# Kernel tuning notes

Measured on AMD Instinct MI355X. Metric: run time of the kernel, lower is better.

The kernel has to match this reference:

```python
import jax, jax.numpy as jnp
import numpy as np

WEIGHTS = (1.0, 2.0, 3.0, 4.0)  # first 4 entries of [1,2,3,4,5,1] for our 4 scales


def _nearest_downsample(pl, H, W):
    # pl: (B,1,H0,W0) int labels; PyTorch F.interpolate nearest: src = floor(dst*H0/H)
    B, _, H0, W0 = pl.shape
    ih = (jnp.arange(H) * H0) // H
    iw = (jnp.arange(W) * W0) // W
    return pl[:, 0][:, ih][:, :, iw]  # (B,H,W)


def _per_class_kl_mean(labels, feat, feat_old, num_class):
    # labels: (N,) int; feat, feat_old: (N,C). Returns (num_class,) per-class mean KL,
    # 0 for absent classes. Labels >= num_class (e.g. 255 ignore) are dropped,
    # matching the original's removal of the 255 class.
    logp = jax.nn.log_softmax(feat, axis=1)
    logq = jax.nn.log_softmax(feat_old, axis=1)
    kl_pix = jnp.sum(jnp.exp(logp) * (logp - logq), axis=1)  # (N,)
    valid = labels < num_class
    seg = jnp.where(valid, labels, num_class)  # invalid -> dummy bucket
    sums = jax.ops.segment_sum(jnp.where(valid, kl_pix, 0.0), seg,
                               num_segments=num_class + 1)[:num_class]
    cnts = jax.ops.segment_sum(valid.astype(feat.dtype), seg,
                               num_segments=num_class + 1)[:num_class]
    return jnp.where(cnts > 0, sums / jnp.maximum(cnts, 1.0), 0.0)


def _forward(pseudo_labels, feats_new, feats_old, num_class, num_old_class):
    cls = jnp.arange(num_class)
    # cl==0 -> num_old/num, 1<=cl<=num_old -> 1, else 0 (absent classes give 0 mean anyway)
    coef = jnp.where(cls == 0, float(num_old_class) / float(num_class),
                     jnp.where(cls <= num_old_class, 1.0, 0.0)).astype(jnp.float32)
    loss = jnp.float32(0.0)
    for idx, (f_new, f_old) in enumerate(zip(feats_new, feats_old)):
        B, C, H, W = f_new.shape
        pl = _nearest_downsample(pseudo_labels, H, W).reshape(-1)  # (B*H*W,)
        feat = jnp.transpose(f_new, (0, 2, 3, 1)).reshape(-1, C)   # (BHW, C)
        feat_old = jnp.transpose(f_old, (0, 2, 3, 1)).reshape(-1, C)
        mean_kl = _per_class_kl_mean(pl, feat, feat_old, num_class)
        loss = loss + WEIGHTS[idx] * jnp.sum(coef * mean_kl)
    return loss


def setup_inputs() -> dict:
    key = jax.random.key(0)
    ks = jax.random.split(key, 9)
    B = 8
    shapes = [(B, 256, 128, 128), (B, 512, 64, 64), (B, 1024, 32, 32), (B, 2048, 16, 16)]
    inp = {}
    inp["pseudo_labels"] = jax.random.randint(ks[0], (B, 1, 512, 512), 0, 21, dtype=jnp.int32)
    for i, s in enumerate(shapes):
        inp[f"feat_new_{i}"] = jax.random.normal(ks[1 + i], s, dtype=jnp.float32)
        inp[f"feat_old_{i}"] = jax.random.normal(ks[5 + i], s, dtype=jnp.float32)
    inp["num_class"] = 21
    inp["num_old_class"] = 15
    return inp


def reference(pseudo_labels, feat_new_0, feat_new_1, feat_new_2, feat_new_3,
              feat_old_0, feat_old_1, feat_old_2, feat_old_3,
              num_class, num_old_class):
    feats_new = (feat_new_0, feat_new_1, feat_new_2, feat_new_3)
    feats_old = (feat_old_0, feat_old_1, feat_old_2, feat_old_3)
    return _forward(pseudo_labels, feats_new, feats_old, num_class, num_old_class)
```

## Files before the change

kernel.cpp:

```cpp
#include <hip/hip_runtime.h>
#include <cstdint>
#include <cstddef>


#define TPB 256

#define P3 2048
#define WS_ZERO_FLOATS (P3 * 3 + 256)

__global__ __launch_bounds__(TPB)
void k0_zero(float* __restrict__ ws) {
    const int i = blockIdx.x * TPB + threadIdx.x;
    if (i < WS_ZERO_FLOATS) ws[i] = 0.f;
}

template<int C, int HW, int W, int F, int PIXT, int CG, int SPLIT>
__device__ __forceinline__ void scale_pass(const float* __restrict__ fn,
                                           const float* __restrict__ fo,
                                           const int* __restrict__ labels,
                                           int ncls, int sc,
                                           float* __restrict__ pZn,
                                           float* __restrict__ pZo,
                                           float* __restrict__ pS,
                                           float* __restrict__ clsSum,
                                           float* __restrict__ clsCnt,
                                           float* red, float* ls, float* lc,
                                           int lb) {
    constexpr int PIXB = 4 * PIXT;
    constexpr int NPB  = (8 * HW) / PIXB;
    constexpr int CH   = C / SPLIT;
    constexpr int IT   = CH / CG;

    const int t  = threadIdx.x;
    const int tx = t % PIXT;
    const int ty = t / PIXT;
    const int pb = lb % NPB;
    const int sp = lb / NPB;

    const int q0 = pb * PIXB;
    const int b  = q0 / HW;
    const int p  = (q0 % HW) + tx * 4;
    const size_t base = (size_t)b * C * HW + p;
    const float* bn = fn + base;
    const float* bo = fo + base;
    const int cbase = sp * CH;

    float zn0=0.f, zn1=0.f, zn2=0.f, zn3=0.f;
    float zo0=0.f, zo1=0.f, zo2=0.f, zo3=0.f;
    float s0 =0.f, s1 =0.f, s2 =0.f, s3 =0.f;

    for (int k = 0; k < IT; ++k) {
        const int c = cbase + k * CG + ty;
        const float4 xn = *(const float4*)(bn + (size_t)c * HW);
        const float4 xo = *(const float4*)(bo + (size_t)c * HW);
        float en, eo;
        en = __expf(xn.x); eo = __expf(xo.x);
        zn0 += en; zo0 += eo; s0 += en * (xn.x - xo.x);
        en = __expf(xn.y); eo = __expf(xo.y);
        zn1 += en; zo1 += eo; s1 += en * (xn.y - xo.y);
        en = __expf(xn.z); eo = __expf(xo.z);
        zn2 += en; zo2 += eo; s2 += en * (xn.z - xo.z);
        en = __expf(xn.w); eo = __expf(xo.w);
        zn3 += en; zo3 += eo; s3 += en * (xn.w - xo.w);
    }

    float* r = red + (size_t)(ty * PIXT + tx) * 12;
    r[0]  = zn0; r[1]  = zo0; r[2]  = s0;
    r[3]  = zn1; r[4]  = zo1; r[5]  = s1;
    r[6]  = zn2; r[7]  = zo2; r[8]  = s2;
    r[9]  = zn3; r[10] = zo3; r[11] = s3;
    if (t < 32) { ls[t] = 0.f; lc[t] = 0.f; }
    __syncthreads();

    for (int i = t; i < PIXB; i += TPB) {
        const int txi = i >> 2;
        const int j   = i & 3;
        float zn = 0.f, zo = 0.f, s = 0.f;
        #pragma unroll
        for (int g = 0; g < CG; ++g) {
            const float* rr = red + (size_t)(g * PIXT + txi) * 12 + j * 3;
            zn += rr[0]; zo += rr[1]; s += rr[2];
        }
        const int q = q0 + i;
        if (SPLIT == 1) {
            const float kl = s / zn - logf(zn) + logf(zo);
            const int pp = q % HW;
            const int h  = pp / W;
            const int w  = pp % W;
            const int lab = labels[b * 262144 + (h * F) * 512 + (w * F)];
            if ((unsigned)lab < (unsigned)ncls) {
                atomicAdd(&ls[lab], kl);
                atomicAdd(&lc[lab], 1.0f);
            }
        } else {
            atomicAdd(&pZn[q], zn);
            atomicAdd(&pZo[q], zo);
            atomicAdd(&pS[q],  s);
        }
    }

    if (SPLIT == 1) {
        __syncthreads();
        if (t < 32) {
            const float cv = lc[t];
            if (cv != 0.f) {
                atomicAdd(&clsSum[sc * 32 + t], ls[t]);
                atomicAdd(&clsCnt[sc * 32 + t], cv);
            }
        }
    }
}

__global__ __launch_bounds__(TPB)
void k1_fused(const float* __restrict__ fn0, const float* __restrict__ fo0,
              const float* __restrict__ fn1, const float* __restrict__ fo1,
              const float* __restrict__ fn2, const float* __restrict__ fo2,
              const float* __restrict__ fn3, const float* __restrict__ fo3,
              const int* __restrict__ labels, const int* __restrict__ pNC,
              float* __restrict__ pZn, float* __restrict__ pZo,
              float* __restrict__ pS,
              float* __restrict__ clsSum, float* __restrict__ clsCnt) {
    __shared__ float red[TPB * 12];
    __shared__ float ls[32], lc[32];
    const int ncls = *pNC;
    const int bb = blockIdx.x;
    if (bb < 512) {
        scale_pass<256, 16384, 128, 4, 64, 4, 1>(fn0, fo0, labels, ncls, 0,
            pZn, pZo, pS, clsSum, clsCnt, red, ls, lc, bb);
    } else if (bb < 768) {
        scale_pass<512, 4096, 64, 8, 32, 8, 1>(fn1, fo1, labels, ncls, 1,
            pZn, pZo, pS, clsSum, clsCnt, red, ls, lc, bb - 512);
    } else if (bb < 1024) {
        scale_pass<1024, 1024, 32, 16, 8, 32, 1>(fn2, fo2, labels, ncls, 2,
            pZn, pZo, pS, clsSum, clsCnt, red, ls, lc, bb - 768);
    } else {
        scale_pass<2048, 256, 16, 32, 8, 32, 4>(fn3, fo3, labels, ncls, 3,
            pZn, pZo, pS, clsSum, clsCnt, red, ls, lc, bb - 1024);
    }
}

__global__ __launch_bounds__(TPB)
void k2_scale3(const int* __restrict__ labels,
               const float* __restrict__ pZn, const float* __restrict__ pZo,
               const float* __restrict__ pS,
               float* __restrict__ clsSum, float* __restrict__ clsCnt,
               const int* __restrict__ pNC) {
    const int ncls = *pNC;
    const int t = threadIdx.x;
    const int q = blockIdx.x * TPB + t;
    __shared__ float ls[32], lc[32];
    if (t < 32) { ls[t] = 0.f; lc[t] = 0.f; }
    __syncthreads();
    const float zn = pZn[q];
    const float zo = pZo[q];
    const float s  = pS[q];
    const float kl = s / zn - logf(zn) + logf(zo);
    const int b  = q / 256;
    const int pp = q % 256;
    const int h  = pp / 16;
    const int w  = pp % 16;
    const int lab = labels[b * 262144 + (h * 32) * 512 + (w * 32)];
    if ((unsigned)lab < (unsigned)ncls) {
        atomicAdd(&ls[lab], kl);
        atomicAdd(&lc[lab], 1.0f);
    }
    __syncthreads();
    if (t < 32 && lc[t] != 0.f) {
        atomicAdd(&clsSum[96 + t], ls[t]);
        atomicAdd(&clsCnt[96 + t], lc[t]);
    }
}

__global__ void k3_finalize(const float* __restrict__ clsSum,
                            const float* __restrict__ clsCnt,
                            const int* __restrict__ pNC,
                            const int* __restrict__ pNOC,
                            float* __restrict__ out) {
    const int t = threadIdx.x;
    const int ncls = *pNC;
    const int nold = *pNOC;
    float acc = 0.f;
    for (int i = t; i < 128; i += 64) {
        const int s_ = i / 32;
        const int c  = i % 32;
        if (c < ncls) {
            const float cnt = clsCnt[i];
            const float sum = clsSum[i];
            const float mean = (cnt > 0.f) ? (sum / cnt) : 0.f;
            const float coef = (c == 0) ? (float)nold / (float)ncls
                                        : ((c <= nold) ? 1.f : 0.f);
            acc += (float)(s_ + 1) * coef * mean;
        }
    }
    #pragma unroll
    for (int off = 32; off > 0; off >>= 1) acc += __shfl_down(acc, off, 64);
    if (t == 0) out[0] = acc;
}

extern "C" void kernel_launch(void* const* d_in, const int* in_sizes, int n_in,
                              void* d_out, int out_size, void* d_ws, size_t ws_size,
                              hipStream_t stream) {
    const int* labels = (const int*)d_in[0];
    const int* pNC;
    const int* pNOC;
    const float* fn[4];
    const float* fo[4];

    if (in_sizes[2] == in_sizes[1]) {
        fn[0] = (const float*)d_in[1]; fo[0] = (const float*)d_in[2];
        fn[1] = (const float*)d_in[3]; fo[1] = (const float*)d_in[4];
        fn[2] = (const float*)d_in[5]; fo[2] = (const float*)d_in[6];
        fn[3] = (const float*)d_in[7]; fo[3] = (const float*)d_in[8];
    } else {
        fn[0] = (const float*)d_in[1]; fn[1] = (const float*)d_in[2];
        fn[2] = (const float*)d_in[3]; fn[3] = (const float*)d_in[4];
        fo[0] = (const float*)d_in[5]; fo[1] = (const float*)d_in[6];
        fo[2] = (const float*)d_in[7]; fo[3] = (const float*)d_in[8];
    }
    pNC  = (const int*)d_in[9];
    pNOC = (const int*)d_in[10];

    float* ws = (float*)d_ws;
    float* pZn = ws;
    float* pZo = ws + P3;
    float* pS  = ws + 2 * P3;
    float* clsSum = ws + 3 * P3;
    float* clsCnt = clsSum + 128;

    k0_zero<<<(WS_ZERO_FLOATS + TPB - 1) / TPB, TPB, 0, stream>>>(ws);
    k1_fused<<<1280, TPB, 0, stream>>>(fn[0], fo[0], fn[1], fo[1],
                                       fn[2], fo[2], fn[3], fo[3],
                                       labels, pNC, pZn, pZo, pS, clsSum, clsCnt);
    k2_scale3<<<P3 / TPB, TPB, 0, stream>>>(labels, pZn, pZo, pS, clsSum, clsCnt, pNC);
    k3_finalize<<<1, 64, 0, stream>>>(clsSum, clsCnt, pNC, pNOC, (float*)d_out);
}
```

Before: 113.1 us.

## Stream feature tiles via global_load_lds double buffering with per-wave channel groups

Rewrites the main reduction pass so each wave asynchronously loads 8-channel by 64-pixel tiles of both feature maps directly into LDS with global_load_lds, double-buffered and synchronised with explicit waitcnt, then consumes them from LDS. The work split changes to per-wave channel groups. Block order is reordered so the heavy small-spatial scales run first, scale 3 uses a 2-way channel split, and the grid grows to 1728 blocks with a 4-blocks-per-CU launch bound. The intent is to keep more memory requests in flight and hide load latency on this bandwidth-bound pass, at the cost of 32KB of LDS per block and hand-written wait counts that could be fragile.

```diff
diff --git a/kernel.cpp b/kernel.cpp
--- a/kernel.cpp
+++ b/kernel.cpp
@@ -4,9 +4,12 @@
 
 
 #define TPB 256
-
 #define P3 2048
 #define WS_ZERO_FLOATS (P3 * 3 + 256)
+
+#define GLL16(gp, lp) __builtin_amdgcn_global_load_lds(                        \
+    (const __attribute__((address_space(1))) unsigned int*)(gp),               \
+    (__attribute__((address_space(3))) unsigned int*)(lp), 16, 0, 0)
 
 __global__ __launch_bounds__(TPB)
 void k0_zero(float* __restrict__ ws) {
@@ -14,7 +17,7 @@
     if (i < WS_ZERO_FLOATS) ws[i] = 0.f;
 }
 
-template<int C, int HW, int W, int F, int PIXT, int CG, int SPLIT>
+template<int C, int HW, int W, int F, int NPGRP, int WCH, int SPLIT>
 __device__ __forceinline__ void scale_pass(const float* __restrict__ fn,
                                            const float* __restrict__ fo,
                                            const int* __restrict__ labels,
@@ -24,94 +27,134 @@
                                            float* __restrict__ pS,
                                            float* __restrict__ clsSum,
                                            float* __restrict__ clsCnt,
-                                           float* red, float* ls, float* lc,
-                                           int lb) {
-    constexpr int PIXB = 4 * PIXT;
-    constexpr int NPB  = (8 * HW) / PIXB;
-    constexpr int CH   = C / SPLIT;
-    constexpr int IT   = CH / CG;
-
-    const int t  = threadIdx.x;
-    const int tx = t % PIXT;
-    const int ty = t / PIXT;
+                                           float* smem, int lb) {
+    constexpr int NPIX = NPGRP * 64;
+    constexpr int NPB  = (8 * HW) / NPIX;
+    constexpr int NCK  = WCH / 8;
+    constexpr int NCHG = 4 / NPGRP;
+
+    const int tid  = threadIdx.x;
+    const int wid  = tid >> 6;
+    const int lane = tid & 63;
     const int pb = lb % NPB;
     const int sp = lb / NPB;
 
-    const int q0 = pb * PIXB;
-    const int b  = q0 / HW;
-    const int p  = (q0 % HW) + tx * 4;
-    const size_t base = (size_t)b * C * HW + p;
-    const float* bn = fn + base;
-    const float* bo = fo + base;
-    const int cbase = sp * CH;
-
-    float zn0=0.f, zn1=0.f, zn2=0.f, zn3=0.f;
-    float zo0=0.f, zo1=0.f, zo2=0.f, zo3=0.f;
-    float s0 =0.f, s1 =0.f, s2 =0.f, s3 =0.f;
-
-    for (int k = 0; k < IT; ++k) {
-        const int c = cbase + k * CG + ty;
-        const float4 xn = *(const float4*)(bn + (size_t)c * HW);
-        const float4 xo = *(const float4*)(bo + (size_t)c * HW);
-        float en, eo;
-        en = __expf(xn.x); eo = __expf(xo.x);
-        zn0 += en; zo0 += eo; s0 += en * (xn.x - xo.x);
-        en = __expf(xn.y); eo = __expf(xo.y);
-        zn1 += en; zo1 += eo; s1 += en * (xn.y - xo.y);
-        en = __expf(xn.z); eo = __expf(xo.z);
-        zn2 += en; zo2 += eo; s2 += en * (xn.z - xo.z);
-        en = __expf(xn.w); eo = __expf(xo.w);
-        zn3 += en; zo3 += eo; s3 += en * (xn.w - xo.w);
-    }
-
-    float* r = red + (size_t)(ty * PIXT + tx) * 12;
-    r[0]  = zn0; r[1]  = zo0; r[2]  = s0;
-    r[3]  = zn1; r[4]  = zo1; r[5]  = s1;
-    r[6]  = zn2; r[7]  = zo2; r[8]  = s2;
-    r[9]  = zn3; r[10] = zo3; r[11] = s3;
-    if (t < 32) { ls[t] = 0.f; lc[t] = 0.f; }
-    __syncthreads();
-
-    for (int i = t; i < PIXB; i += TPB) {
-        const int txi = i >> 2;
-        const int j   = i & 3;
+    const int pg = wid % NPGRP;
+    const int cg = wid / NPGRP;
+
+    const int blkpix0 = pb * NPIX;
+    const int p0 = blkpix0 + pg * 64;
+    const int b  = p0 / HW;
+    const int ppix = p0 % HW;
+    const int ch0w = sp * (NCHG * WCH) + cg * WCH;
+
+    const int cst = lane >> 4;
+    const int qq  = lane & 15;
+
+    const float* gn = fn + ((size_t)b * C + ch0w + cst) * HW + ppix + qq * 4;
+    const float* go = fo + ((size_t)b * C + ch0w + cst) * HW + ppix + qq * 4;
+
+    float* wbuf = smem + wid * 2048;
+
+    float zn0=0.f,zn1=0.f,zn2=0.f,zn3=0.f;
+    float zo0=0.f,zo1=0.f,zo2=0.f,zo3=0.f;
+    float sA0=0.f,sA1=0.f,sA2=0.f,sA3=0.f;
+
+#define STAGE(k_, d_) do {                                                     \
+        const size_t co_ = (size_t)((k_) * 8) * HW;                            \
+        float* lb0_ = wbuf + (d_) * 1024;                                      \
+        GLL16(gn + co_,              lb0_);                                    \
+        GLL16(gn + co_ + 4 * (size_t)HW, lb0_ + 256);                          \
+        GLL16(go + co_,              lb0_ + 512);                              \
+        GLL16(go + co_ + 4 * (size_t)HW, lb0_ + 768);                          \
+    } while (0)
+
+#define ACC(nv, ov, i_) { const float en_=__expf(nv), eo_=__expf(ov);          \
+        zn##i_ += en_; zo##i_ += eo_; sA##i_ += en_ * ((nv) - (ov)); }
+
+#define CONSUME(d_) do {                                                       \
+        const float* nb_ = wbuf + (d_) * 1024;                                 \
+        const float* ob_ = nb_ + 512;                                          \
+        const float4 n0_ = *(const float4*)(nb_ + (2*cst  )*64 + qq*4);        \
+        const float4 n1_ = *(const float4*)(nb_ + (2*cst+1)*64 + qq*4);        \
+        const float4 o0_ = *(const float4*)(ob_ + (2*cst  )*64 + qq*4);        \
+        const float4 o1_ = *(const float4*)(ob_ + (2*cst+1)*64 + qq*4);        \
+        ACC(n0_.x,o0_.x,0) ACC(n0_.y,o0_.y,1) ACC(n0_.z,o0_.z,2) ACC(n0_.w,o0_.w,3) \
+        ACC(n1_.x,o1_.x,0) ACC(n1_.y,o1_.y,1) ACC(n1_.z,o1_.z,2) ACC(n1_.w,o1_.w,3) \
+    } while (0)
+
+    STAGE(0, 0);
+    STAGE(1, 1);
+    for (int k = 0; k < NCK - 1; ++k) {
+        asm volatile("s_waitcnt vmcnt(4)" ::: "memory");
+        __builtin_amdgcn_sched_barrier(0);
+        CONSUME(k & 1);
+        asm volatile("s_waitcnt lgkmcnt(0)" ::: "memory");
+        __builtin_amdgcn_sched_barrier(0);
+        if (k + 2 < NCK) STAGE(k + 2, k & 1);
+    }
+    asm volatile("s_waitcnt vmcnt(0)" ::: "memory");
+    __builtin_amdgcn_sched_barrier(0);
+    CONSUME((NCK - 1) & 1);
+
+#undef STAGE
+#undef ACC
+#undef CONSUME
+
+    __syncthreads();
+    float* red = smem;
+    float* r = red + tid * 12;
+    r[0]=zn0; r[1]=zn1; r[2]=zn2;  r[3]=zn3;
+    r[4]=zo0; r[5]=zo1; r[6]=zo2;  r[7]=zo3;
+    r[8]=sA0; r[9]=sA1; r[10]=sA2; r[11]=sA3;
+    float* ls = smem + 3072;
+    float* lc = smem + 3104;
+    if (tid < 32) { ls[tid] = 0.f; lc[tid] = 0.f; }
+    __syncthreads();
+
+    for (int i = tid; i < NPIX; i += TPB) {
+        const int Q = i >> 2, j = i & 3;
+        const int pgq = (NPGRP == 2) ? (Q >> 4) : 0;
+        const int ql = Q & 15;
         float zn = 0.f, zo = 0.f, s = 0.f;
         #pragma unroll
-        for (int g = 0; g < CG; ++g) {
-            const float* rr = red + (size_t)(g * PIXT + txi) * 12 + j * 3;
-            zn += rr[0]; zo += rr[1]; s += rr[2];
-        }
-        const int q = q0 + i;
+        for (int cgi = 0; cgi < NCHG; ++cgi) {
+            #pragma unroll
+            for (int g = 0; g < 4; ++g) {
+                const float* rr = red + ((pgq + cgi * NPGRP) * 64 + g * 16 + ql) * 12;
+                zn += rr[j]; zo += rr[4 + j]; s += rr[8 + j];
+            }
+        }
+        const int qg = blkpix0 + i;
         if (SPLIT == 1) {
             const float kl = s / zn - logf(zn) + logf(zo);
-            const int pp = q % HW;
-            const int h  = pp / W;
-            const int w  = pp % W;
+            const int pp = qg % HW;
+            const int h = pp / W, w = pp % W;
             const int lab = labels[b * 262144 + (h * F) * 512 + (w * F)];
             if ((unsigned)lab < (unsigned)ncls) {
                 atomicAdd(&ls[lab], kl);
                 atomicAdd(&lc[lab], 1.0f);
             }
         } else {
-            atomicAdd(&pZn[q], zn);
-            atomicAdd(&pZo[q], zo);
-            atomicAdd(&pS[q],  s);
+            atomicAdd(&pZn[qg], zn);
+            atomicAdd(&pZo[qg], zo);
+            atomicAdd(&pS[qg],  s);
         }
     }
 
     if (SPLIT == 1) {
         __syncthreads();
-        if (t < 32) {
-            const float cv = lc[t];
+        if (tid < 32) {
+            const float cv = lc[tid];
             if (cv != 0.f) {
-                atomicAdd(&clsSum[sc * 32 + t], ls[t]);
-                atomicAdd(&clsCnt[sc * 32 + t], cv);
+                atomicAdd(&clsSum[sc * 32 + tid], ls[tid]);
+                atomicAdd(&clsCnt[sc * 32 + tid], cv);
             }
         }
     }
 }
 
-__global__ __launch_bounds__(TPB)
+__global__ __launch_bounds__(TPB, 4)
 void k1_fused(const float* __restrict__ fn0, const float* __restrict__ fo0,
               const float* __restrict__ fn1, const float* __restrict__ fo1,
               const float* __restrict__ fn2, const float* __restrict__ fo2,
@@ -120,22 +163,21 @@
               float* __restrict__ pZn, float* __restrict__ pZo,
               float* __restrict__ pS,
               float* __restrict__ clsSum, float* __restrict__ clsCnt) {
-    __shared__ float red[TPB * 12];
-    __shared__ float ls[32], lc[32];
+    __shared__ float smem[8192];
     const int ncls = *pNC;
     const int bb = blockIdx.x;
-    if (bb < 512) {
-        scale_pass<256, 16384, 128, 4, 64, 4, 1>(fn0, fo0, labels, ncls, 0,
-            pZn, pZo, pS, clsSum, clsCnt, red, ls, lc, bb);
-    } else if (bb < 768) {
-        scale_pass<512, 4096, 64, 8, 32, 8, 1>(fn1, fo1, labels, ncls, 1,
-            pZn, pZo, pS, clsSum, clsCnt, red, ls, lc, bb - 512);
-    } else if (bb < 1024) {
-        scale_pass<1024, 1024, 32, 16, 8, 32, 1>(fn2, fo2, labels, ncls, 2,
-            pZn, pZo, pS, clsSum, clsCnt, red, ls, lc, bb - 768);
+    if (bb < 128) {
+        scale_pass<1024, 1024, 32, 16, 1, 256, 1>(fn2, fo2, labels, ncls, 2,
+            pZn, pZo, pS, clsSum, clsCnt, smem, bb);
+    } else if (bb < 192) {
+        scale_pass<2048, 256, 16, 32, 1, 256, 2>(fn3, fo3, labels, ncls, 3,
+            pZn, pZo, pS, clsSum, clsCnt, smem, bb - 128);
+    } else if (bb < 704) {
+        scale_pass<512, 4096, 64, 8, 1, 128, 1>(fn1, fo1, labels, ncls, 1,
+            pZn, pZo, pS, clsSum, clsCnt, smem, bb - 192);
     } else {
-        scale_pass<2048, 256, 16, 32, 8, 32, 4>(fn3, fo3, labels, ncls, 3,
-            pZn, pZo, pS, clsSum, clsCnt, red, ls, lc, bb - 1024);
+        scale_pass<256, 16384, 128, 4, 2, 128, 1>(fn0, fo0, labels, ncls, 0,
+            pZn, pZo, pS, clsSum, clsCnt, smem, bb - 704);
     }
 }
 
@@ -201,8 +243,6 @@
                               void* d_out, int out_size, void* d_ws, size_t ws_size,
                               hipStream_t stream) {
     const int* labels = (const int*)d_in[0];
-    const int* pNC;
-    const int* pNOC;
     const float* fn[4];
     const float* fo[4];
 
@@ -217,8 +257,8 @@
         fo[0] = (const float*)d_in[5]; fo[1] = (const float*)d_in[6];
         fo[2] = (const float*)d_in[7]; fo[3] = (const float*)d_in[8];
     }
-    pNC  = (const int*)d_in[9];
-    pNOC = (const int*)d_in[10];
+    const int* pNC  = (const int*)d_in[9];
+    const int* pNOC = (const int*)d_in[10];
 
     float* ws = (float*)d_ws;
     float* pZn = ws;
@@ -228,7 +268,7 @@
     float* clsCnt = clsSum + 128;
 
     k0_zero<<<(WS_ZERO_FLOATS + TPB - 1) / TPB, TPB, 0, stream>>>(ws);
-    k1_fused<<<1280, TPB, 0, stream>>>(fn[0], fo[0], fn[1], fo[1],
+    k1_fused<<<1728, TPB, 0, stream>>>(fn[0], fo[0], fn[1], fo[1],
                                        fn[2], fo[2], fn[3], fo[3],
                                        labels, pNC, pZn, pZo, pS, clsSum, clsCnt);
     k2_scale3<<<P3 / TPB, TPB, 0, stream>>>(labels, pZn, pZo, pS, clsSum, clsCnt, pNC);
```

Result: faster. 107.8 us (-4.7%).

## Use uniform 256-pixel x 256-channel tiles with split-channel atomics for scales 1-3

Applied to the files above, without the earlier changes.

Every scale now uses the same block tile: 256 pixels by 256 channels, four waves of 64 channels each, with loads unrolled four channels deep. Scales 1 and 2 now split channels across blocks too, and partial softmax sums go to a larger global partial buffer through atomics. A generalized second kernel then finishes scales 1-3, and launch bounds request 4 blocks per CU. The aim is uniform memory-level parallelism and fewer reduction stalls, at the cost of more global atomics and a larger workspace to zero.

```diff
diff --git a/kernel.cpp b/kernel.cpp
--- a/kernel.cpp
+++ b/kernel.cpp
@@ -4,9 +4,10 @@
 
 
 #define TPB 256
-
-#define P3 2048
-#define WS_ZERO_FLOATS (P3 * 3 + 256)
+#define NPART 43008
+#define WS_ZERO_FLOATS (NPART * 3 + 256)
+
+#define LD4(p) (*(const float4*)(p))
 
 __global__ __launch_bounds__(TPB)
 void k0_zero(float* __restrict__ ws) {
@@ -14,104 +15,100 @@
     if (i < WS_ZERO_FLOATS) ws[i] = 0.f;
 }
 
-template<int C, int HW, int W, int F, int PIXT, int CG, int SPLIT>
+template<int C, int HW, int W, int F, bool FIN>
 __device__ __forceinline__ void scale_pass(const float* __restrict__ fn,
                                            const float* __restrict__ fo,
                                            const int* __restrict__ labels,
-                                           int ncls, int sc,
+                                           int ncls, int pOff,
                                            float* __restrict__ pZn,
                                            float* __restrict__ pZo,
                                            float* __restrict__ pS,
                                            float* __restrict__ clsSum,
                                            float* __restrict__ clsCnt,
-                                           float* red, float* ls, float* lc,
-                                           int lb) {
-    constexpr int PIXB = 4 * PIXT;
-    constexpr int NPB  = (8 * HW) / PIXB;
-    constexpr int CH   = C / SPLIT;
-    constexpr int IT   = CH / CG;
-
-    const int t  = threadIdx.x;
-    const int tx = t % PIXT;
-    const int ty = t / PIXT;
-    const int pb = lb % NPB;
-    const int sp = lb / NPB;
-
-    const int q0 = pb * PIXB;
-    const int b  = q0 / HW;
-    const int p  = (q0 % HW) + tx * 4;
-    const size_t base = (size_t)b * C * HW + p;
-    const float* bn = fn + base;
-    const float* bo = fo + base;
-    const int cbase = sp * CH;
-
-    float zn0=0.f, zn1=0.f, zn2=0.f, zn3=0.f;
-    float zo0=0.f, zo1=0.f, zo2=0.f, zo3=0.f;
-    float s0 =0.f, s1 =0.f, s2 =0.f, s3 =0.f;
-
-    for (int k = 0; k < IT; ++k) {
-        const int c = cbase + k * CG + ty;
-        const float4 xn = *(const float4*)(bn + (size_t)c * HW);
-        const float4 xo = *(const float4*)(bo + (size_t)c * HW);
-        float en, eo;
-        en = __expf(xn.x); eo = __expf(xo.x);
-        zn0 += en; zo0 += eo; s0 += en * (xn.x - xo.x);
-        en = __expf(xn.y); eo = __expf(xo.y);
-        zn1 += en; zo1 += eo; s1 += en * (xn.y - xo.y);
-        en = __expf(xn.z); eo = __expf(xo.z);
-        zn2 += en; zo2 += eo; s2 += en * (xn.z - xo.z);
-        en = __expf(xn.w); eo = __expf(xo.w);
-        zn3 += en; zo3 += eo; s3 += en * (xn.w - xo.w);
-    }
-
-    float* r = red + (size_t)(ty * PIXT + tx) * 12;
-    r[0]  = zn0; r[1]  = zo0; r[2]  = s0;
-    r[3]  = zn1; r[4]  = zo1; r[5]  = s1;
-    r[6]  = zn2; r[7]  = zo2; r[8]  = s2;
-    r[9]  = zn3; r[10] = zo3; r[11] = s3;
-    if (t < 32) { ls[t] = 0.f; lc[t] = 0.f; }
+                                           float* smem, int lb) {
+    constexpr int NPXB = (8 * HW) / 256;
+
+    const int tid  = threadIdx.x;
+    const int wid  = tid >> 6;
+    const int lane = tid & 63;
+    const int pxb = lb % NPXB;
+    const int cb  = lb / NPXB;
+
+    const int q0  = pxb * 256;
+    const int b   = q0 / HW;
+    const int px0 = q0 % HW;
+    const int c0  = cb * 256 + wid * 64;
+
+    const float* pn = fn + ((size_t)b * C + c0) * HW + px0 + 4 * lane;
+    const float* po = fo + ((size_t)b * C + c0) * HW + px0 + 4 * lane;
+
+    float zn0=0.f,zn1=0.f,zn2=0.f,zn3=0.f;
+    float zo0=0.f,zo1=0.f,zo2=0.f,zo3=0.f;
+    float sA0=0.f,sA1=0.f,sA2=0.f,sA3=0.f;
+
+#define ACC(nv, ov, i_) { const float en_=__expf(nv), eo_=__expf(ov);          \
+        zn##i_ += en_; zo##i_ += eo_; sA##i_ += en_ * ((nv) - (ov)); }
+#define ACCQ(a_, b_) { ACC(a_.x,b_.x,0) ACC(a_.y,b_.y,1)                        \
+                       ACC(a_.z,b_.z,2) ACC(a_.w,b_.w,3) }
+
+    for (int k = 0; k < 64; k += 4) {
+        const size_t o0 = (size_t)(k + 0) * HW;
+        const size_t o1 = (size_t)(k + 1) * HW;
+        const size_t o2 = (size_t)(k + 2) * HW;
+        const size_t o3 = (size_t)(k + 3) * HW;
+        const float4 xn0 = LD4(pn + o0), xn1 = LD4(pn + o1);
+        const float4 xn2 = LD4(pn + o2), xn3 = LD4(pn + o3);
+        const float4 xo0 = LD4(po + o0), xo1 = LD4(po + o1);
+        const float4 xo2 = LD4(po + o2), xo3 = LD4(po + o3);
+        ACCQ(xn0, xo0) ACCQ(xn1, xo1) ACCQ(xn2, xo2) ACCQ(xn3, xo3)
+    }
+#undef ACC
+#undef ACCQ
+
+    float* lacc = smem;
+    float* r = lacc + wid * 768 + lane * 12;
+    r[0]=zn0; r[1]=zo0; r[2]=sA0;
+    r[3]=zn1; r[4]=zo1; r[5]=sA1;
+    r[6]=zn2; r[7]=zo2; r[8]=sA2;
+    r[9]=zn3; r[10]=zo3; r[11]=sA3;
+    float* ls = smem + 3072;
+    float* lc = smem + 3104;
+    if (tid < 32) { ls[tid] = 0.f; lc[tid] = 0.f; }
     __syncthreads();
 
-    for (int i = t; i < PIXB; i += TPB) {
-        const int txi = i >> 2;
-        const int j   = i & 3;
-        float zn = 0.f, zo = 0.f, s = 0.f;
-        #pragma unroll
-        for (int g = 0; g < CG; ++g) {
-            const float* rr = red + (size_t)(g * PIXT + txi) * 12 + j * 3;
-            zn += rr[0]; zo += rr[1]; s += rr[2];
+    float zn = 0.f, zo = 0.f, s = 0.f;
+    #pragma unroll
+    for (int w = 0; w < 4; ++w) {
+        const float* rr = lacc + w * 768 + tid * 3;
+        zn += rr[0]; zo += rr[1]; s += rr[2];
+    }
+
+    if (FIN) {
+        const float kl = s / zn - logf(zn) + logf(zo);
+        const int pp = px0 + tid;
+        const int h = pp / W, w = pp % W;
+        const int lab = labels[b * 262144 + (h * F) * 512 + (w * F)];
+        if ((unsigned)lab < (unsigned)ncls) {
+            atomicAdd(&ls[lab], kl);
+            atomicAdd(&lc[lab], 1.0f);
         }
-        const int q = q0 + i;
-        if (SPLIT == 1) {
-            const float kl = s / zn - logf(zn) + logf(zo);
-            const int pp = q % HW;
-            const int h  = pp / W;
-            const int w  = pp % W;
-            const int lab = labels[b * 262144 + (h * F) * 512 + (w * F)];
-            if ((unsigned)lab < (unsigned)ncls) {
-                atomicAdd(&ls[lab], kl);
-                atomicAdd(&lc[lab], 1.0f);
-            }
-        } else {
-            atomicAdd(&pZn[q], zn);
-            atomicAdd(&pZo[q], zo);
-            atomicAdd(&pS[q],  s);
-        }
-    }
-
-    if (SPLIT == 1) {
         __syncthreads();
-        if (t < 32) {
-            const float cv = lc[t];
+        if (tid < 32) {
+            const float cv = lc[tid];
             if (cv != 0.f) {
-                atomicAdd(&clsSum[sc * 32 + t], ls[t]);
-                atomicAdd(&clsCnt[sc * 32 + t], cv);
+                atomicAdd(&clsSum[tid], ls[tid]);
+                atomicAdd(&clsCnt[tid], cv);
             }
         }
-    }
-}
-
-__global__ __launch_bounds__(TPB)
+    } else {
+        const int g = pOff + q0 + tid;
+        atomicAdd(&pZn[g], zn);
+        atomicAdd(&pZo[g], zo);
+        atomicAdd(&pS[g],  s);
+    }
+}
+
+__global__ __launch_bounds__(TPB, 4)
 void k1_fused(const float* __restrict__ fn0, const float* __restrict__ fo0,
               const float* __restrict__ fn1, const float* __restrict__ fo1,
               const float* __restrict__ fn2, const float* __restrict__ fo2,
@@ -120,54 +117,60 @@
               float* __restrict__ pZn, float* __restrict__ pZo,
               float* __restrict__ pS,
               float* __restrict__ clsSum, float* __restrict__ clsCnt) {
-    __shared__ float red[TPB * 12];
-    __shared__ float ls[32], lc[32];
+    __shared__ float smem[3136];
     const int ncls = *pNC;
     const int bb = blockIdx.x;
     if (bb < 512) {
-        scale_pass<256, 16384, 128, 4, 64, 4, 1>(fn0, fo0, labels, ncls, 0,
-            pZn, pZo, pS, clsSum, clsCnt, red, ls, lc, bb);
+        scale_pass<256, 16384, 128, 4, true>(fn0, fo0, labels, ncls, 0,
+            pZn, pZo, pS, clsSum, clsCnt, smem, bb);
     } else if (bb < 768) {
-        scale_pass<512, 4096, 64, 8, 32, 8, 1>(fn1, fo1, labels, ncls, 1,
-            pZn, pZo, pS, clsSum, clsCnt, red, ls, lc, bb - 512);
-    } else if (bb < 1024) {
-        scale_pass<1024, 1024, 32, 16, 8, 32, 1>(fn2, fo2, labels, ncls, 2,
-            pZn, pZo, pS, clsSum, clsCnt, red, ls, lc, bb - 768);
+        scale_pass<512, 4096, 64, 8, false>(fn1, fo1, labels, ncls, 0,
+            pZn, pZo, pS, clsSum, clsCnt, smem, bb - 512);
+    } else if (bb < 896) {
+        scale_pass<1024, 1024, 32, 16, false>(fn2, fo2, labels, ncls, 32768,
+            pZn, pZo, pS, clsSum, clsCnt, smem, bb - 768);
     } else {
-        scale_pass<2048, 256, 16, 32, 8, 32, 4>(fn3, fo3, labels, ncls, 3,
-            pZn, pZo, pS, clsSum, clsCnt, red, ls, lc, bb - 1024);
+        scale_pass<2048, 256, 16, 32, false>(fn3, fo3, labels, ncls, 40960,
+            pZn, pZo, pS, clsSum, clsCnt, smem, bb - 896);
     }
 }
 
 __global__ __launch_bounds__(TPB)
-void k2_scale3(const int* __restrict__ labels,
+void k2_finish(const int* __restrict__ labels,
                const float* __restrict__ pZn, const float* __restrict__ pZo,
                const float* __restrict__ pS,
                float* __restrict__ clsSum, float* __restrict__ clsCnt,
                const int* __restrict__ pNC) {
     const int ncls = *pNC;
     const int t = threadIdx.x;
-    const int q = blockIdx.x * TPB + t;
+    const int i = blockIdx.x * TPB + t;
+
+    int sc, q, HW, W, F;
+    if (i < 32768)      { sc = 1; q = i;          HW = 4096; W = 64; F = 8;  }
+    else if (i < 40960) { sc = 2; q = i - 32768;  HW = 1024; W = 32; F = 16; }
+    else                { sc = 3; q = i - 40960;  HW = 256;  W = 16; F = 32; }
+
     __shared__ float ls[32], lc[32];
     if (t < 32) { ls[t] = 0.f; lc[t] = 0.f; }
     __syncthreads();
-    const float zn = pZn[q];
-    const float zo = pZo[q];
-    const float s  = pS[q];
+
+    const float zn = pZn[i];
+    const float zo = pZo[i];
+    const float s  = pS[i];
     const float kl = s / zn - logf(zn) + logf(zo);
-    const int b  = q / 256;
-    const int pp = q % 256;
-    const int h  = pp / 16;
-    const int w  = pp % 16;
-    const int lab = labels[b * 262144 + (h * 32) * 512 + (w * 32)];
+    const int b  = q / HW;
+    const int pp = q % HW;
+    const int h  = pp / W;
+    const int w  = pp % W;
+    const int lab = labels[b * 262144 + (h * F) * 512 + (w * F)];
     if ((unsigned)lab < (unsigned)ncls) {
         atomicAdd(&ls[lab], kl);
         atomicAdd(&lc[lab], 1.0f);
     }
     __syncthreads();
     if (t < 32 && lc[t] != 0.f) {
-        atomicAdd(&clsSum[96 + t], ls[t]);
-        atomicAdd(&clsCnt[96 + t], lc[t]);
+        atomicAdd(&clsSum[sc * 32 + t], ls[t]);
+        atomicAdd(&clsCnt[sc * 32 + t], lc[t]);
     }
 }
 
@@ -201,8 +204,6 @@
                               void* d_out, int out_size, void* d_ws, size_t ws_size,
                               hipStream_t stream) {
     const int* labels = (const int*)d_in[0];
-    const int* pNC;
-    const int* pNOC;
     const float* fn[4];
     const float* fo[4];
 
@@ -217,20 +218,21 @@
         fo[0] = (const float*)d_in[5]; fo[1] = (const float*)d_in[6];
         fo[2] = (const float*)d_in[7]; fo[3] = (const float*)d_in[8];
     }
-    pNC  = (const int*)d_in[9];
-    pNOC = (const int*)d_in[10];
+    const int* pNC  = (const int*)d_in[9];
+    const int* pNOC = (const int*)d_in[10];
 
     float* ws = (float*)d_ws;
     float* pZn = ws;
-    float* pZo = ws + P3;
-    float* pS  = ws + 2 * P3;
-    float* clsSum = ws + 3 * P3;
+    float* pZo = ws + NPART;
+    float* pS  = ws + 2 * (size_t)NPART;
+    float* clsSum = ws + 3 * (size_t)NPART;
     float* clsCnt = clsSum + 128;
 
     k0_zero<<<(WS_ZERO_FLOATS + TPB - 1) / TPB, TPB, 0, stream>>>(ws);
-    k1_fused<<<1280, TPB, 0, stream>>>(fn[0], fo[0], fn[1], fo[1],
-                                       fn[2], fo[2], fn[3], fo[3],
-                                       labels, pNC, pZn, pZo, pS, clsSum, clsCnt);
-    k2_scale3<<<P3 / TPB, TPB, 0, stream>>>(labels, pZn, pZo, pS, clsSum, clsCnt, pNC);
+    k1_fused<<<960, TPB, 0, stream>>>(fn[0], fo[0], fn[1], fo[1],
+                                      fn[2], fo[2], fn[3], fo[3],
+                                      labels, pNC, pZn, pZo, pS, clsSum, clsCnt);
+    k2_finish<<<NPART / TPB, TPB, 0, stream>>>(labels, pZn, pZo, pS,
+                                               clsSum, clsCnt, pNC);
     k3_finalize<<<1, 64, 0, stream>>>(clsSum, clsCnt, pNC, pNOC, (float*)d_out);
 }
```

After: 117.1 us. 1.04x slower.
